# Optimization experiments

Hardware: AMD Instinct MI355X
Metric: run time of the kernel (lower is better)

The kernel has to match this reference:

```python
import jax, jax.numpy as jnp
import numpy as np

N_DIM = 256
NHIDDEN = 256
NLAYERS = 4
LAMDA = 0.5
ALPHA = 0.1
MODAL_WEIGHT = 1.0
N_SPEAKERS = 2
B_DIA = 100   # number of dialogues
L_DIA = 40    # utterances per dialogue
N_UTT = B_DIA * L_DIA


def _cos_sim_blocks(x, B, L):
    # per-dialogue cosine-similarity blocks: x [N, d] -> [B, L, L]
    xb = x.reshape(B, L, -1)
    xn = xb / jnp.linalg.norm(xb, axis=-1, keepdims=True)
    cos = jnp.einsum('bid,bjd->bij', xn, xn) * 0.99999
    return 1.0 - jnp.arccos(cos) / jnp.pi


def setup_inputs() -> dict:
    key = jax.random.key(0)
    ks = jax.random.split(key, 8)
    return {
        'a': jax.random.normal(ks[0], (N_UTT, N_DIM), jnp.float32),
        'v': jax.random.normal(ks[1], (N_UTT, N_DIM), jnp.float32),
        'l': jax.random.normal(ks[2], (N_UTT, N_DIM), jnp.float32),
        'qmask': jax.random.uniform(ks[3], (L_DIA, B_DIA, N_SPEAKERS), jnp.float32),
        'spk_emb': jax.random.normal(ks[4], (N_SPEAKERS, N_DIM), jnp.float32) * 0.02,
        'W0': jax.random.normal(ks[5], (N_DIM, NHIDDEN), jnp.float32) / np.sqrt(N_DIM).astype(np.float32),
        'b0': jnp.zeros((NHIDDEN,), jnp.float32),
        'Wconvs': jax.random.normal(ks[6], (NLAYERS, NHIDDEN, NHIDDEN), jnp.float32) / np.sqrt(NHIDDEN).astype(np.float32),
        'dia_len_each': L_DIA,
        'n_dialogues': B_DIA,
    }


def reference(a, v, l, qmask, spk_emb, W0, b0, Wconvs, dia_len_each, n_dialogues):
    B, L = n_dialogues, dia_len_each
    N = B * L
    M = 3  # modals 'avl'

    # --- speaker embedding added to text modality (use_speaker) ---
    # torch.cat([qmask[:x, i, :] for i, x in enumerate(dia_len)]) with equal lengths
    q = jnp.transpose(qmask, (1, 0, 2)).reshape(N, -1)   # [N, n_speakers]
    spk_idx = jnp.argmax(q, axis=-1)                      # [N]
    l = l + spk_emb[spk_idx]

    feats = [a, v, l]
    normed = [f / jnp.linalg.norm(f, axis=-1, keepdims=True) for f in feats]

    # --- create_big_adj: block-diag per-modal cosine-sim blocks + cross-modal diagonals ---
    adj = jnp.zeros((M * N, M * N), jnp.float32)
    idx = jnp.arange(N).reshape(B, L)
    rows = idx[:, :, None]   # [B, L, 1]
    cols = idx[:, None, :]   # [B, 1, L]
    ar = jnp.arange(N)
    for m in range(M):
        sim = _cos_sim_blocks(feats[m], B, L)            # [B, L, L]
        adj = adj.at[m * N + rows, m * N + cols].set(sim)
    for m in range(M):
        for n in range(M):
            if m == n:
                continue
            cs = jnp.sum(normed[m] * normed[n], axis=-1) * 0.99999
            dia_sim = 1.0 - jnp.arccos(cs) / jnp.pi
            adj = adj.at[m * N + ar, n * N + ar].set(dia_sim * MODAL_WEIGHT)
    d = jnp.sum(adj, axis=1)
    dinv = d ** -0.5
    adj = adj * dinv[:, None] * dinv[None, :]            # D^-1/2 A D^-1/2

    # --- GCNII_lyc propagation (eval mode, variant=False, no dropout) ---
    x = jnp.concatenate(feats, axis=0)                   # [3N, n_dim]
    h0 = jax.nn.relu(x @ W0 + b0)
    h = h0
    for i in range(NLAYERS):
        theta = float(np.log(LAMDA / (i + 1) + 1.0))
        hi = adj @ h
        support = (1.0 - ALPHA) * hi + ALPHA * h0
        h = jax.nn.relu(theta * (support @ Wconvs[i]) + (1.0 - theta) * support)
    feat = jnp.concatenate([x, h], axis=-1)              # use_residue

    # regroup modalities per utterance: [N, 3*(n_dim+nhidden)]
    out = jnp.concatenate([feat[:N], feat[N:2 * N], feat[2 * N:3 * N]], axis=-1)
    return out
```

## Files before the change

kernel.cpp:

```cpp
#include <hip/hip_runtime.h>
#include <hip/hip_bf16.h>

#define N_UTT 4000
#define NDIM 256
#define B_DIA 100
#define L_DIA 40
#define NLAYERS 4

typedef __attribute__((ext_vector_type(8))) short short8;
typedef __attribute__((ext_vector_type(4))) float f32x4;

union bfpk4 { __hip_bfloat16 h[4]; uint2 u; };

static __device__ __forceinline__ float bf2f(__hip_bfloat16 h) {
  union { float f; unsigned u; } x;
  x.u = ((unsigned)*(unsigned short*)&h) << 16;
  return x.f;
}

__global__ void k_wt(const float* __restrict__ W0, const float* __restrict__ Wc,
                     __hip_bfloat16* __restrict__ Wt) {
  int k0 = blockIdx.x * 64, n0 = blockIdx.y * 64, g = blockIdx.z;
  int t = threadIdx.x;
  const float* src = (g == 0) ? W0 : (Wc + (g - 1) * NDIM * NDIM);
  __shared__ float tile[64][65];
  #pragma unroll
  for (int it = 0; it < 16; it++) {
    int e = t + 256 * it;
    int row = e >> 6, col = e & 63;
    tile[row][col] = src[(k0 + row) * NDIM + n0 + col];
  }
  __syncthreads();
  #pragma unroll
  for (int it = 0; it < 16; it++) {
    int e = t + 256 * it;
    int row = e >> 6, col = e & 63;
    Wt[(g * NDIM + n0 + row) * NDIM + k0 + col] = __float2bfloat16(tile[col][row]);
  }
}

__global__ __launch_bounds__(512, 1) void k_main(
    const float* __restrict__ a, const float* __restrict__ v,
    const float* __restrict__ lf, const float* __restrict__ qmask,
    const float* __restrict__ spk, const float* __restrict__ b0,
    const __hip_bfloat16* __restrict__ Wt, float* __restrict__ out) {
  __shared__ __hip_bfloat16 xls[3][L_DIA][264];
  __shared__ __hip_bfloat16 hls[3][NDIM][L_DIA];
  __shared__ __hip_bfloat16 sext[3][L_DIA][136];
  __shared__ float invn[120];
  __shared__ float dinv[120];
  __shared__ float psum[120][4];

  int b = blockIdx.x;
  int t = threadIdx.x;
  int w = t >> 6, ln = t & 63;
  int l15 = ln & 15, lk = (ln >> 4) * 8;
  const float inv_pi = 0.31830988618379067f;

  int arows[3], cols[2];
  #pragma unroll
  for (int rt = 0; rt < 3; rt++) {
    int rr_ = rt * 16 + l15;
    arows[rt] = (rr_ < L_DIA) ? rr_ : (L_DIA - 1);
  }
  #pragma unroll
  for (int c = 0; c < 2; c++) cols[c] = w * 32 + c * 16 + l15;

  {
    unsigned int* sz = (unsigned int*)&sext[0][0][0];
    #pragma unroll
    for (int e = t; e < 3 * L_DIA * 136 / 2; e += 512) sz[e] = 0u;
  }
  for (int e = t; e < 120 * 64; e += 512) {
    int r = e >> 6, c4 = e & 63;
    int m = r / L_DIA, p = r - m * L_DIA;
    int i = b * L_DIA + p;
    float4 val;
    if (m == 0)      val = ((const float4*)a)[i * 64 + c4];
    else if (m == 1) val = ((const float4*)v)[i * 64 + c4];
    else {
      val = ((const float4*)lf)[i * 64 + c4];
      float q0 = qmask[(p * B_DIA + b) * 2 + 0];
      float q1 = qmask[(p * B_DIA + b) * 2 + 1];
      int s = (q1 > q0) ? 1 : 0;
      float4 sv = ((const float4*)spk)[s * 64 + c4];
      val.x += sv.x; val.y += sv.y; val.z += sv.z; val.w += sv.w;
    }
    ((float4*)out)[i * 384 + m * 128 + c4] = val;
    bfpk4 pk;
    pk.h[0] = __float2bfloat16(val.x); pk.h[1] = __float2bfloat16(val.y);
    pk.h[2] = __float2bfloat16(val.z); pk.h[3] = __float2bfloat16(val.w);
    *(uint2*)&xls[m][p][c4 * 4] = pk.u;
  }
  __syncthreads();

  if (t < 480) {
    int r = t >> 2, q4 = t & 3;
    int m = r / L_DIA, p = r - m * L_DIA;
    float s = 0.f;
    #pragma unroll
    for (int jj = 0; jj < 8; jj++) {
      short8 vv = *(const short8*)&xls[m][p][q4 * 64 + jj * 8];
      #pragma unroll
      for (int e = 0; e < 8; e++) {
        union { float f; unsigned u; } x;
        x.u = ((unsigned)(unsigned short)vv[e]) << 16;
        s += x.f * x.f;
      }
    }
    psum[r][q4] = s;
  }
  __syncthreads();
  if (t < 120) invn[t] = rsqrtf(psum[t][0] + psum[t][1] + psum[t][2] + psum[t][3]);
  __syncthreads();

  if (w < 3) {
    int mA = w;
    f32x4 sacc[3][3];
    #pragma unroll
    for (int rt = 0; rt < 3; rt++)
      #pragma unroll
      for (int ct = 0; ct < 3; ct++) sacc[rt][ct] = (f32x4){0.f,0.f,0.f,0.f};
    #pragma unroll
    for (int k0 = 0; k0 < NDIM; k0 += 32) {
      short8 fr[3];
      #pragma unroll
      for (int rt = 0; rt < 3; rt++)
        fr[rt] = *(const short8*)&xls[mA][arows[rt]][k0 + lk];
      #pragma unroll
      for (int rt = 0; rt < 3; rt++)
        #pragma unroll
        for (int ct = 0; ct < 3; ct++)
          sacc[rt][ct] = __builtin_amdgcn_mfma_f32_16x16x32_bf16(fr[rt], fr[ct], sacc[rt][ct], 0, 0, 0);
    }
    #pragma unroll
    for (int rt = 0; rt < 3; rt++)
      #pragma unroll
      for (int ct = 0; ct < 3; ct++)
        #pragma unroll
        for (int rr = 0; rr < 4; rr++) {
          int row = rt * 16 + (ln >> 4) * 4 + rr;
          int col = ct * 16 + l15;
          if (row < L_DIA && col < L_DIA) {
            float cs = sacc[rt][ct][rr] * invn[mA * 40 + row] * invn[mA * 40 + col] * 0.99999f;
            cs = fminf(fmaxf(cs, -1.f), 1.f);
            sext[mA][row][col] = __float2bfloat16(1.f - acosf(cs) * inv_pi);
          }
        }
  } else if (w < 6) {
    int pi = w - 3;
    int mA = (pi == 2) ? 1 : 0, mB = (pi == 0) ? 1 : 2;
    int slotA = (pi == 0) ? 40 : 80, slotB = (pi == 2) ? 80 : 40;
    f32x4 dacc[3];
    #pragma unroll
    for (int rt = 0; rt < 3; rt++) dacc[rt] = (f32x4){0.f,0.f,0.f,0.f};
    #pragma unroll
    for (int k0 = 0; k0 < NDIM; k0 += 32) {
      short8 frA[3], frB[3];
      #pragma unroll
      for (int rt = 0; rt < 3; rt++) {
        frA[rt] = *(const short8*)&xls[mA][arows[rt]][k0 + lk];
        frB[rt] = *(const short8*)&xls[mB][arows[rt]][k0 + lk];
      }
      #pragma unroll
      for (int rt = 0; rt < 3; rt++)
        dacc[rt] = __builtin_amdgcn_mfma_f32_16x16x32_bf16(frA[rt], frB[rt], dacc[rt], 0, 0, 0);
    }
    #pragma unroll
    for (int rt = 0; rt < 3; rt++)
      #pragma unroll
      for (int rr = 0; rr < 4; rr++) {
        int row = rt * 16 + (ln >> 4) * 4 + rr;
        if (l15 == ((ln >> 4) * 4 + rr) && row < L_DIA) {
          float cs = dacc[rt][rr] * invn[mA * 40 + row] * invn[mB * 40 + row] * 0.99999f;
          cs = fminf(fmaxf(cs, -1.f), 1.f);
          __hip_bfloat16 vv = __float2bfloat16(1.f - acosf(cs) * inv_pi);
          sext[mA][row][slotA + row] = vv;
          sext[mB][row][slotB + row] = vv;
        }
      }
  }
  __syncthreads();

  if (t < 120) {
    int m = t / 40, p = t - m * 40;
    float d = 0.f;
    #pragma unroll 10
    for (int q = 0; q < 40; q++) d += bf2f(sext[m][p][q]);
    d += bf2f(sext[m][p][40 + p]) + bf2f(sext[m][p][80 + p]);
    dinv[t] = rsqrtf(d);
  }
  __syncthreads();
  for (int e = t; e < 5040; e += 512) {
    if (e < 4800) {
      int m = e / 1600, rem = e - m * 1600;
      int p = rem / 40, q = rem - p * 40;
      sext[m][p][q] = __float2bfloat16(
          bf2f(sext[m][p][q]) * 0.9f * dinv[m * 40 + p] * dinv[m * 40 + q]);
    } else {
      int idx = e - 4800;
      int m = idx / 80, j = idx - m * 80;
      int which = j / 40, p = j - which * 40;
      int pmx = which ? ((m == 2) ? 1 : 2) : ((m == 0) ? 1 : 0);
      int k = 40 * (1 + which) + p;
      sext[m][p][k] = __float2bfloat16(
          bf2f(sext[m][p][k]) * 0.9f * dinv[m * 40 + p] * dinv[pmx * 40 + p]);
    }
  }
  __syncthreads();

  uint2 h0r[9][2];
  {
    f32x4 acc[9][2];
    #pragma unroll
    for (int s = 0; s < 9; s++)
      #pragma unroll
      for (int c = 0; c < 2; c++) acc[s][c] = (f32x4){0.f,0.f,0.f,0.f};
    #pragma unroll
    for (int k0 = 0; k0 < NDIM; k0 += 32) {
      short8 bfw[2];
      #pragma unroll
      for (int c = 0; c < 2; c++)
        bfw[c] = *(const short8*)&Wt[cols[c] * NDIM + k0 + lk];
      short8 af[9];
      #pragma unroll
      for (int s = 0; s < 9; s++)
        af[s] = *(const short8*)&xls[s / 3][arows[s % 3]][k0 + lk];
      #pragma unroll
      for (int s = 0; s < 9; s++)
        #pragma unroll
        for (int c = 0; c < 2; c++)
          acc[s][c] = __builtin_amdgcn_mfma_f32_16x16x32_bf16(af[s], bfw[c], acc[s][c], 0, 0, 0);
    }
    #pragma unroll
    for (int s = 0; s < 9; s++) {
      int p0 = (s % 3) * 16 + (ln >> 4) * 4;
      #pragma unroll
      for (int c = 0; c < 2; c++) {
        float bias = b0[cols[c]];
        bfpk4 pk;
        #pragma unroll
        for (int rr = 0; rr < 4; rr++)
          pk.h[rr] = __float2bfloat16(fmaxf(acc[s][c][rr] + bias, 0.f));
        h0r[s][c] = pk.u;
        if (p0 < L_DIA) *(uint2*)&hls[s / 3][cols[c]][p0] = pk.u;
      }
    }
  }
  __syncthreads();

  const float thetas[NLAYERS] = {0.40546510810816438f, 0.22314355131420976f,
                                 0.15415067982725836f, 0.11778303565638346f};
  #pragma unroll
  for (int li = 0; li < NLAYERS; li++) {
    float th = thetas[li], onemt = 1.f - th;
    const __hip_bfloat16* Wl = Wt + (li + 1) * NDIM * NDIM;

    {
      f32x4 acc[9][2];
      #pragma unroll
      for (int s = 0; s < 9; s++)
        #pragma unroll
        for (int c = 0; c < 2; c++) acc[s][c] = (f32x4){0.f,0.f,0.f,0.f};
      #pragma unroll
      for (int j = 0; j < 4; j++) {
        short8 bfv[3][2];
        #pragma unroll
        for (int mm = 0; mm < 3; mm++) {
          int pm0 = (mm == 0) ? 1 : 0, pm1 = (mm == 2) ? 1 : 2;
          int kk = j * 32 + lk;
          int srcm, brow;
          if (kk < 40)       { srcm = mm;  brow = kk; }
          else if (kk < 80)  { srcm = pm0; brow = kk - 40; }
          else if (kk < 120) { srcm = pm1; brow = kk - 80; }
          else               { srcm = pm1; brow = 32; }
          #pragma unroll
          for (int c = 0; c < 2; c++)
            bfv[mm][c] = *(const short8*)&hls[srcm][cols[c]][brow];
        }
        short8 af[9];
        #pragma unroll
        for (int s = 0; s < 9; s++)
          af[s] = *(const short8*)&sext[s / 3][arows[s % 3]][j * 32 + lk];
        #pragma unroll
        for (int s = 0; s < 9; s++)
          #pragma unroll
          for (int c = 0; c < 2; c++)
            acc[s][c] = __builtin_amdgcn_mfma_f32_16x16x32_bf16(af[s], bfv[s / 3][c], acc[s][c], 0, 0, 0);
      }
      #pragma unroll
      for (int s = 0; s < 9; s++) {
        int p0 = (s % 3) * 16 + (ln >> 4) * 4;
        #pragma unroll
        for (int c = 0; c < 2; c++) {
          bfpk4 h0p; h0p.u = h0r[s][c];
          if (p0 < L_DIA) {
            #pragma unroll
            for (int rr = 0; rr < 4; rr++)
              xls[s / 3][p0 + rr][cols[c]] =
                  __float2bfloat16(acc[s][c][rr] + 0.1f * bf2f(h0p.h[rr]));
          }
        }
      }
    }
    __syncthreads();

    {
      f32x4 o[9][2];
      #pragma unroll
      for (int s = 0; s < 9; s++)
        #pragma unroll
        for (int c = 0; c < 2; c++) o[s][c] = (f32x4){0.f,0.f,0.f,0.f};
      #pragma unroll
      for (int k0 = 0; k0 < NDIM; k0 += 32) {
        short8 bfw[2];
        #pragma unroll
        for (int c = 0; c < 2; c++)
          bfw[c] = *(const short8*)&Wl[cols[c] * NDIM + k0 + lk];
        short8 af[9];
        #pragma unroll
        for (int s = 0; s < 9; s++)
          af[s] = *(const short8*)&xls[s / 3][arows[s % 3]][k0 + lk];
        #pragma unroll
        for (int s = 0; s < 9; s++)
          #pragma unroll
          for (int c = 0; c < 2; c++)
            o[s][c] = __builtin_amdgcn_mfma_f32_16x16x32_bf16(af[s], bfw[c], o[s][c], 0, 0, 0);
      }
      #pragma unroll
      for (int s = 0; s < 9; s++) {
        int m = s / 3;
        int p0 = (s % 3) * 16 + (ln >> 4) * 4;
        if (p0 >= L_DIA) continue;
        #pragma unroll
        for (int c = 0; c < 2; c++) {
          int col = cols[c];
          if (li < NLAYERS - 1) {
            bfpk4 pk;
            #pragma unroll
            for (int rr = 0; rr < 4; rr++) {
              float supv = bf2f(xls[m][p0 + rr][col]);
              pk.h[rr] = __float2bfloat16(fmaxf(th * o[s][c][rr] + onemt * supv, 0.f));
            }
            *(uint2*)&hls[m][col][p0] = pk.u;
          } else {
            #pragma unroll
            for (int rr = 0; rr < 4; rr++) {
              float supv = bf2f(xls[m][p0 + rr][col]);
              out[(b * L_DIA + p0 + rr) * 1536 + m * 512 + 256 + col] =
                  fmaxf(th * o[s][c][rr] + onemt * supv, 0.f);
            }
          }
        }
      }
    }
    __syncthreads();
  }
}

extern "C" void kernel_launch(void* const* d_in, const int* in_sizes, int n_in,
                              void* d_out, int out_size, void* d_ws, size_t ws_size,
                              hipStream_t stream) {
  const float* a     = (const float*)d_in[0];
  const float* v     = (const float*)d_in[1];
  const float* lf    = (const float*)d_in[2];
  const float* qmask = (const float*)d_in[3];
  const float* spk   = (const float*)d_in[4];
  const float* W0    = (const float*)d_in[5];
  const float* b0    = (const float*)d_in[6];
  const float* Wc    = (const float*)d_in[7];
  float* out = (float*)d_out;

  __hip_bfloat16* Wt = (__hip_bfloat16*)d_ws;

  k_wt<<<dim3(4, 4, 5), 256, 0, stream>>>(W0, Wc, Wt);
  k_main<<<B_DIA, 512, 0, stream>>>(a, v, lf, qmask, spk, b0, Wt, out);
}
```

Before: 63.63 us.

## Split row-tiles across two wave groups with 64-column tiles per wave

```diff
diff --git a/kernel.cpp b/kernel.cpp
--- a/kernel.cpp
+++ b/kernel.cpp
@@ -57,14 +57,20 @@
   int l15 = ln & 15, lk = (ln >> 4) * 8;
   const float inv_pi = 0.31830988618379067f;
 
-  int arows[3], cols[2];
+  int sgrp = w >> 2;
+  int cw = w & 3;
+  int sbase = sgrp ? 5 : 0;
+  int scnt  = sgrp ? 4 : 5;
+  int mlist0 = sgrp ? 1 : 0, mlist1 = sgrp ? 2 : 1;
+
+  int arows[3], cols[4];
   #pragma unroll
   for (int rt = 0; rt < 3; rt++) {
     int rr_ = rt * 16 + l15;
     arows[rt] = (rr_ < L_DIA) ? rr_ : (L_DIA - 1);
   }
   #pragma unroll
-  for (int c = 0; c < 2; c++) cols[c] = w * 32 + c * 16 + l15;
+  for (int c = 0; c < 4; c++) cols[c] = cw * 64 + c * 16 + l15;
 
   {
     unsigned int* sz = (unsigned int*)&sext[0][0][0];
@@ -209,40 +215,46 @@
   }
   __syncthreads();
 
-  uint2 h0r[9][2];
+  uint2 h0r[5][4];
   {
-    f32x4 acc[9][2];
-    #pragma unroll
-    for (int s = 0; s < 9; s++)
-      #pragma unroll
-      for (int c = 0; c < 2; c++) acc[s][c] = (f32x4){0.f,0.f,0.f,0.f};
+    f32x4 acc[5][4];
+    #pragma unroll
+    for (int si = 0; si < 5; si++)
+      #pragma unroll
+      for (int c = 0; c < 4; c++) acc[si][c] = (f32x4){0.f,0.f,0.f,0.f};
     #pragma unroll
     for (int k0 = 0; k0 < NDIM; k0 += 32) {
-      short8 bfw[2];
-      #pragma unroll
-      for (int c = 0; c < 2; c++)
+      short8 bfw[4];
+      #pragma unroll
+      for (int c = 0; c < 4; c++)
         bfw[c] = *(const short8*)&Wt[cols[c] * NDIM + k0 + lk];
-      short8 af[9];
-      #pragma unroll
-      for (int s = 0; s < 9; s++)
-        af[s] = *(const short8*)&xls[s / 3][arows[s % 3]][k0 + lk];
-      #pragma unroll
-      for (int s = 0; s < 9; s++)
-        #pragma unroll
-        for (int c = 0; c < 2; c++)
-          acc[s][c] = __builtin_amdgcn_mfma_f32_16x16x32_bf16(af[s], bfw[c], acc[s][c], 0, 0, 0);
-    }
-    #pragma unroll
-    for (int s = 0; s < 9; s++) {
+      short8 af[5];
+      #pragma unroll
+      for (int si = 0; si < 5; si++)
+        if (si < scnt) {
+          int s = sbase + si;
+          af[si] = *(const short8*)&xls[s / 3][arows[s % 3]][k0 + lk];
+        }
+      #pragma unroll
+      for (int si = 0; si < 5; si++)
+        if (si < scnt)
+          #pragma unroll
+          for (int c = 0; c < 4; c++)
+            acc[si][c] = __builtin_amdgcn_mfma_f32_16x16x32_bf16(af[si], bfw[c], acc[si][c], 0, 0, 0);
+    }
+    #pragma unroll
+    for (int si = 0; si < 5; si++) {
+      if (si >= scnt) continue;
+      int s = sbase + si;
       int p0 = (s % 3) * 16 + (ln >> 4) * 4;
       #pragma unroll
-      for (int c = 0; c < 2; c++) {
+      for (int c = 0; c < 4; c++) {
         float bias = b0[cols[c]];
         bfpk4 pk;
         #pragma unroll
         for (int rr = 0; rr < 4; rr++)
-          pk.h[rr] = __float2bfloat16(fmaxf(acc[s][c][rr] + bias, 0.f));
-        h0r[s][c] = pk.u;
+          pk.h[rr] = __float2bfloat16(fmaxf(acc[si][c][rr] + bias, 0.f));
+        h0r[si][c] = pk.u;
         if (p0 < L_DIA) *(uint2*)&hls[s / 3][cols[c]][p0] = pk.u;
       }
     }
@@ -255,50 +267,64 @@
   for (int li = 0; li < NLAYERS; li++) {
     float th = thetas[li], onemt = 1.f - th;
     const __hip_bfloat16* Wl = Wt + (li + 1) * NDIM * NDIM;
+    uint2 supb[5][4];
 
     {
-      f32x4 acc[9][2];
-      #pragma unroll
-      for (int s = 0; s < 9; s++)
-        #pragma unroll
-        for (int c = 0; c < 2; c++) acc[s][c] = (f32x4){0.f,0.f,0.f,0.f};
+      f32x4 acc[5][4];
+      #pragma unroll
+      for (int si = 0; si < 5; si++)
+        #pragma unroll
+        for (int c = 0; c < 4; c++) acc[si][c] = (f32x4){0.f,0.f,0.f,0.f};
       #pragma unroll
       for (int j = 0; j < 4; j++) {
-        short8 bfv[3][2];
-        #pragma unroll
-        for (int mm = 0; mm < 3; mm++) {
+        int kk = j * 32 + lk;
+        short8 bfv[2][4];
+        #pragma unroll
+        for (int mi = 0; mi < 2; mi++) {
+          int mm = mi ? mlist1 : mlist0;
           int pm0 = (mm == 0) ? 1 : 0, pm1 = (mm == 2) ? 1 : 2;
-          int kk = j * 32 + lk;
           int srcm, brow;
           if (kk < 40)       { srcm = mm;  brow = kk; }
           else if (kk < 80)  { srcm = pm0; brow = kk - 40; }
           else if (kk < 120) { srcm = pm1; brow = kk - 80; }
           else               { srcm = pm1; brow = 32; }
           #pragma unroll
-          for (int c = 0; c < 2; c++)
-            bfv[mm][c] = *(const short8*)&hls[srcm][cols[c]][brow];
-        }
-        short8 af[9];
-        #pragma unroll
-        for (int s = 0; s < 9; s++)
-          af[s] = *(const short8*)&sext[s / 3][arows[s % 3]][j * 32 + lk];
-        #pragma unroll
-        for (int s = 0; s < 9; s++)
+          for (int c = 0; c < 4; c++)
+            bfv[mi][c] = *(const short8*)&hls[srcm][cols[c]][brow];
+        }
+        short8 af[5];
+        #pragma unroll
+        for (int si = 0; si < 5; si++)
+          if (si < scnt) {
+            int s = sbase + si;
+            af[si] = *(const short8*)&sext[s / 3][arows[s % 3]][j * 32 + lk];
+          }
+        #pragma unroll
+        for (int si = 0; si < 5; si++)
+          if (si < scnt) {
+            int mi = (((sbase + si) / 3) == mlist0) ? 0 : 1;
+            #pragma unroll
+            for (int c = 0; c < 4; c++)
+              acc[si][c] = __builtin_amdgcn_mfma_f32_16x16x32_bf16(af[si], bfv[mi][c], acc[si][c], 0, 0, 0);
+          }
+      }
+      #pragma unroll
+      for (int si = 0; si < 5; si++) {
+        if (si >= scnt) continue;
+        int s = sbase + si, m = s / 3;
+        int p0 = (s % 3) * 16 + (ln >> 4) * 4;
+        #pragma unroll
+        for (int c = 0; c < 4; c++) {
+          bfpk4 h0p; h0p.u = h0r[si][c];
+          bfpk4 pk;
           #pragma unroll
-          for (int c = 0; c < 2; c++)
-            acc[s][c] = __builtin_amdgcn_mfma_f32_16x16x32_bf16(af[s], bfv[s / 3][c], acc[s][c], 0, 0, 0);
-      }
-      #pragma unroll
-      for (int s = 0; s < 9; s++) {
-        int p0 = (s % 3) * 16 + (ln >> 4) * 4;
-        #pragma unroll
-        for (int c = 0; c < 2; c++) {
-          bfpk4 h0p; h0p.u = h0r[s][c];
+          for (int rr = 0; rr < 4; rr++)
+            pk.h[rr] = __float2bfloat16(acc[si][c][rr] + 0.1f * bf2f(h0p.h[rr]));
+          supb[si][c] = pk.u;
           if (p0 < L_DIA) {
             #pragma unroll
             for (int rr = 0; rr < 4; rr++)
-              xls[s / 3][p0 + rr][cols[c]] =
-                  __float2bfloat16(acc[s][c][rr] + 0.1f * bf2f(h0p.h[rr]));
+              xls[m][p0 + rr][cols[c]] = pk.h[rr];
           }
         }
       }
@@ -306,50 +332,52 @@
     __syncthreads();
 
     {
-      f32x4 o[9][2];
-      #pragma unroll
-      for (int s = 0; s < 9; s++)
-        #pragma unroll
-        for (int c = 0; c < 2; c++) o[s][c] = (f32x4){0.f,0.f,0.f,0.f};
+      f32x4 o[5][4];
+      #pragma unroll
+      for (int si = 0; si < 5; si++)
+        #pragma unroll
+        for (int c = 0; c < 4; c++) o[si][c] = (f32x4){0.f,0.f,0.f,0.f};
       #pragma unroll
       for (int k0 = 0; k0 < NDIM; k0 += 32) {
-        short8 bfw[2];
-        #pragma unroll
-        for (int c = 0; c < 2; c++)
+        short8 bfw[4];
+        #pragma unroll
+        for (int c = 0; c < 4; c++)
           bfw[c] = *(const short8*)&Wl[cols[c] * NDIM + k0 + lk];
-        short8 af[9];
-        #pragma unroll
-        for (int s = 0; s < 9; s++)
-          af[s] = *(const short8*)&xls[s / 3][arows[s % 3]][k0 + lk];
-        #pragma unroll
-        for (int s = 0; s < 9; s++)
-          #pragma unroll
-          for (int c = 0; c < 2; c++)
-            o[s][c] = __builtin_amdgcn_mfma_f32_16x16x32_bf16(af[s], bfw[c], o[s][c], 0, 0, 0);
-      }
-      #pragma unroll
-      for (int s = 0; s < 9; s++) {
-        int m = s / 3;
+        short8 af[5];
+        #pragma unroll
+        for (int si = 0; si < 5; si++)
+          if (si < scnt) {
+            int s = sbase + si;
+            af[si] = *(const short8*)&xls[s / 3][arows[s % 3]][k0 + lk];
+          }
+        #pragma unroll
+        for (int si = 0; si < 5; si++)
+          if (si < scnt)
+            #pragma unroll
+            for (int c = 0; c < 4; c++)
+              o[si][c] = __builtin_amdgcn_mfma_f32_16x16x32_bf16(af[si], bfw[c], o[si][c], 0, 0, 0);
+      }
+      #pragma unroll
+      for (int si = 0; si < 5; si++) {
+        if (si >= scnt) continue;
+        int s = sbase + si, m = s / 3;
         int p0 = (s % 3) * 16 + (ln >> 4) * 4;
         if (p0 >= L_DIA) continue;
         #pragma unroll
-        for (int c = 0; c < 2; c++) {
-          int col = cols[c];
+        for (int c = 0; c < 4; c++) {
+          bfpk4 sp; sp.u = supb[si][c];
           if (li < NLAYERS - 1) {
             bfpk4 pk;
             #pragma unroll
-            for (int rr = 0; rr < 4; rr++) {
-              float supv = bf2f(xls[m][p0 + rr][col]);
-              pk.h[rr] = __float2bfloat16(fmaxf(th * o[s][c][rr] + onemt * supv, 0.f));
-            }
-            *(uint2*)&hls[m][col][p0] = pk.u;
+            for (int rr = 0; rr < 4; rr++)
+              pk.h[rr] = __float2bfloat16(
+                  fmaxf(th * o[si][c][rr] + onemt * bf2f(sp.h[rr]), 0.f));
+            *(uint2*)&hls[m][cols[c]][p0] = pk.u;
           } else {
             #pragma unroll
-            for (int rr = 0; rr < 4; rr++) {
-              float supv = bf2f(xls[m][p0 + rr][col]);
-              out[(b * L_DIA + p0 + rr) * 1536 + m * 512 + 256 + col] =
-                  fmaxf(th * o[s][c][rr] + onemt * supv, 0.f);
-            }
+            for (int rr = 0; rr < 4; rr++)
+              out[(b * L_DIA + p0 + rr) * 1536 + m * 512 + 256 + cols[c]] =
+                  fmaxf(th * o[si][c][rr] + onemt * bf2f(sp.h[rr]), 0.f);
           }
         }
       }
```

After: 138.5 us. 2.18x slower.

## Use 12 waves per block, splitting work by modality and column group

Applied to the files above, without the earlier changes.

```diff
diff --git a/kernel.cpp b/kernel.cpp
--- a/kernel.cpp
+++ b/kernel.cpp
@@ -6,6 +6,7 @@
 #define B_DIA 100
 #define L_DIA 40
 #define NLAYERS 4
+#define NT 768
 
 typedef __attribute__((ext_vector_type(8))) short short8;
 typedef __attribute__((ext_vector_type(4))) float f32x4;
@@ -39,7 +40,7 @@
   }
 }
 
-__global__ __launch_bounds__(512, 1) void k_main(
+__global__ __launch_bounds__(NT, 3) void k_main(
     const float* __restrict__ a, const float* __restrict__ v,
     const float* __restrict__ lf, const float* __restrict__ qmask,
     const float* __restrict__ spk, const float* __restrict__ b0,
@@ -55,23 +56,28 @@
   int t = threadIdx.x;
   int w = t >> 6, ln = t & 63;
   int l15 = ln & 15, lk = (ln >> 4) * 8;
+  int hi4 = (ln >> 4) * 4;
   const float inv_pi = 0.31830988618379067f;
 
-  int arows[3], cols[2];
+  int mg = w >> 2;
+  int cg = w & 3;
+  int pm0 = (mg == 0) ? 1 : 0;
+  int pm1 = (mg == 2) ? 1 : 2;
+
+  int arows[3], cols[4];
   #pragma unroll
   for (int rt = 0; rt < 3; rt++) {
     int rr_ = rt * 16 + l15;
     arows[rt] = (rr_ < L_DIA) ? rr_ : (L_DIA - 1);
   }
   #pragma unroll
-  for (int c = 0; c < 2; c++) cols[c] = w * 32 + c * 16 + l15;
+  for (int c = 0; c < 4; c++) cols[c] = cg * 64 + c * 16 + l15;
 
   {
     unsigned int* sz = (unsigned int*)&sext[0][0][0];
-    #pragma unroll
-    for (int e = t; e < 3 * L_DIA * 136 / 2; e += 512) sz[e] = 0u;
-  }
-  for (int e = t; e < 120 * 64; e += 512) {
+    for (int e = t; e < 3 * L_DIA * 136 / 2; e += NT) sz[e] = 0u;
+  }
+  for (int e = t; e < 120 * 64; e += NT) {
     int r = e >> 6, c4 = e & 63;
     int m = r / L_DIA, p = r - m * L_DIA;
     int i = b * L_DIA + p;
@@ -139,7 +145,7 @@
       for (int ct = 0; ct < 3; ct++)
         #pragma unroll
         for (int rr = 0; rr < 4; rr++) {
-          int row = rt * 16 + (ln >> 4) * 4 + rr;
+          int row = rt * 16 + hi4 + rr;
           int col = ct * 16 + l15;
           if (row < L_DIA && col < L_DIA) {
             float cs = sacc[rt][ct][rr] * invn[mA * 40 + row] * invn[mA * 40 + col] * 0.99999f;
@@ -170,8 +176,8 @@
     for (int rt = 0; rt < 3; rt++)
       #pragma unroll
       for (int rr = 0; rr < 4; rr++) {
-        int row = rt * 16 + (ln >> 4) * 4 + rr;
-        if (l15 == ((ln >> 4) * 4 + rr) && row < L_DIA) {
+        int row = rt * 16 + hi4 + rr;
+        if (l15 == (hi4 + rr) && row < L_DIA) {
           float cs = dacc[rt][rr] * invn[mA * 40 + row] * invn[mB * 40 + row] * 0.99999f;
           cs = fminf(fmaxf(cs, -1.f), 1.f);
           __hip_bfloat16 vv = __float2bfloat16(1.f - acosf(cs) * inv_pi);
@@ -191,7 +197,7 @@
     dinv[t] = rsqrtf(d);
   }
   __syncthreads();
-  for (int e = t; e < 5040; e += 512) {
+  for (int e = t; e < 5040; e += NT) {
     if (e < 4800) {
       int m = e / 1600, rem = e - m * 1600;
       int p = rem / 40, q = rem - p * 40;
@@ -209,41 +215,41 @@
   }
   __syncthreads();
 
-  uint2 h0r[9][2];
+  uint2 h0r[3][4];
   {
-    f32x4 acc[9][2];
-    #pragma unroll
-    for (int s = 0; s < 9; s++)
-      #pragma unroll
-      for (int c = 0; c < 2; c++) acc[s][c] = (f32x4){0.f,0.f,0.f,0.f};
+    f32x4 acc[3][4];
+    #pragma unroll
+    for (int rt = 0; rt < 3; rt++)
+      #pragma unroll
+      for (int c = 0; c < 4; c++) acc[rt][c] = (f32x4){0.f,0.f,0.f,0.f};
     #pragma unroll
     for (int k0 = 0; k0 < NDIM; k0 += 32) {
-      short8 bfw[2];
-      #pragma unroll
-      for (int c = 0; c < 2; c++)
+      short8 bfw[4];
+      #pragma unroll
+      for (int c = 0; c < 4; c++)
         bfw[c] = *(const short8*)&Wt[cols[c] * NDIM + k0 + lk];
-      short8 af[9];
-      #pragma unroll
-      for (int s = 0; s < 9; s++)
-        af[s] = *(const short8*)&xls[s / 3][arows[s % 3]][k0 + lk];
-      #pragma unroll
-      for (int s = 0; s < 9; s++)
-        #pragma unroll
-        for (int c = 0; c < 2; c++)
-          acc[s][c] = __builtin_amdgcn_mfma_f32_16x16x32_bf16(af[s], bfw[c], acc[s][c], 0, 0, 0);
-    }
-    #pragma unroll
-    for (int s = 0; s < 9; s++) {
-      int p0 = (s % 3) * 16 + (ln >> 4) * 4;
-      #pragma unroll
-      for (int c = 0; c < 2; c++) {
+      short8 af[3];
+      #pragma unroll
+      for (int rt = 0; rt < 3; rt++)
+        af[rt] = *(const short8*)&xls[mg][arows[rt]][k0 + lk];
+      #pragma unroll
+      for (int rt = 0; rt < 3; rt++)
+        #pragma unroll
+        for (int c = 0; c < 4; c++)
+          acc[rt][c] = __builtin_amdgcn_mfma_f32_16x16x32_bf16(af[rt], bfw[c], acc[rt][c], 0, 0, 0);
+    }
+    #pragma unroll
+    for (int rt = 0; rt < 3; rt++) {
+      int p0 = rt * 16 + hi4;
+      #pragma unroll
+      for (int c = 0; c < 4; c++) {
         float bias = b0[cols[c]];
         bfpk4 pk;
         #pragma unroll
         for (int rr = 0; rr < 4; rr++)
-          pk.h[rr] = __float2bfloat16(fmaxf(acc[s][c][rr] + bias, 0.f));
-        h0r[s][c] = pk.u;
-        if (p0 < L_DIA) *(uint2*)&hls[s / 3][cols[c]][p0] = pk.u;
+          pk.h[rr] = __float2bfloat16(fmaxf(acc[rt][c][rr] + bias, 0.f));
+        h0r[rt][c] = pk.u;
+        if (p0 < L_DIA) *(uint2*)&hls[mg][cols[c]][p0] = pk.u;
       }
     }
   }
@@ -257,48 +263,44 @@
     const __hip_bfloat16* Wl = Wt + (li + 1) * NDIM * NDIM;
 
     {
-      f32x4 acc[9][2];
-      #pragma unroll
-      for (int s = 0; s < 9; s++)
-        #pragma unroll
-        for (int c = 0; c < 2; c++) acc[s][c] = (f32x4){0.f,0.f,0.f,0.f};
+      f32x4 acc[3][4];
+      #pragma unroll
+      for (int rt = 0; rt < 3; rt++)
+        #pragma unroll
+        for (int c = 0; c < 4; c++) acc[rt][c] = (f32x4){0.f,0.f,0.f,0.f};
       #pragma unroll
       for (int j = 0; j < 4; j++) {
-        short8 bfv[3][2];
-        #pragma unroll
-        for (int mm = 0; mm < 3; mm++) {
-          int pm0 = (mm == 0) ? 1 : 0, pm1 = (mm == 2) ? 1 : 2;
-          int kk = j * 32 + lk;
-          int srcm, brow;
-          if (kk < 40)       { srcm = mm;  brow = kk; }
-          else if (kk < 80)  { srcm = pm0; brow = kk - 40; }
-          else if (kk < 120) { srcm = pm1; brow = kk - 80; }
-          else               { srcm = pm1; brow = 32; }
+        int kk = j * 32 + lk;
+        int srcm, brow;
+        if (kk < 40)       { srcm = mg;  brow = kk; }
+        else if (kk < 80)  { srcm = pm0; brow = kk - 40; }
+        else if (kk < 120) { srcm = pm1; brow = kk - 80; }
+        else               { srcm = pm1; brow = 32; }
+        short8 bfv[4];
+        #pragma unroll
+        for (int c = 0; c < 4; c++)
+          bfv[c] = *(const short8*)&hls[srcm][cols[c]][brow];
+        short8 af[3];
+        #pragma unroll
+        for (int rt = 0; rt < 3; rt++)
+          af[rt] = *(const short8*)&sext[mg][arows[rt]][j * 32 + lk];
+        #pragma unroll
+        for (int rt = 0; rt < 3; rt++)
           #pragma unroll
-          for (int c = 0; c < 2; c++)
-            bfv[mm][c] = *(const short8*)&hls[srcm][cols[c]][brow];
-        }
-        short8 af[9];
-        #pragma unroll
-        for (int s = 0; s < 9; s++)
-          af[s] = *(const short8*)&sext[s / 3][arows[s % 3]][j * 32 + lk];
-        #pragma unroll
-        for (int s = 0; s < 9; s++)
+          for (int c = 0; c < 4; c++)
+            acc[rt][c] = __builtin_amdgcn_mfma_f32_16x16x32_bf16(af[rt], bfv[c], acc[rt][c], 0, 0, 0);
+      }
+      #pragma unroll
+      for (int rt = 0; rt < 3; rt++) {
+        int p0 = rt * 16 + hi4;
+        if (p0 < L_DIA) {
           #pragma unroll
-          for (int c = 0; c < 2; c++)
-            acc[s][c] = __builtin_amdgcn_mfma_f32_16x16x32_bf16(af[s], bfv[s / 3][c], acc[s][c], 0, 0, 0);
-      }
-      #pragma unroll
-      for (int s = 0; s < 9; s++) {
-        int p0 = (s % 3) * 16 + (ln >> 4) * 4;
-        #pragma unroll
-        for (int c = 0; c < 2; c++) {
-          bfpk4 h0p; h0p.u = h0r[s][c];
-          if (p0 < L_DIA) {
+          for (int c = 0; c < 4; c++) {
+            bfpk4 h0p; h0p.u = h0r[rt][c];
             #pragma unroll
             for (int rr = 0; rr < 4; rr++)
-              xls[s / 3][p0 + rr][cols[c]] =
-                  __float2bfloat16(acc[s][c][rr] + 0.1f * bf2f(h0p.h[rr]));
+              xls[mg][p0 + rr][cols[c]] =
+                  __float2bfloat16(acc[rt][c][rr] + 0.1f * bf2f(h0p.h[rr]));
           }
         }
       }
@@ -306,49 +308,48 @@
     __syncthreads();
 
     {
-      f32x4 o[9][2];
-      #pragma unroll
-      for (int s = 0; s < 9; s++)
-        #pragma unroll
-        for (int c = 0; c < 2; c++) o[s][c] = (f32x4){0.f,0.f,0.f,0.f};
+      f32x4 o[3][4];
+      #pragma unroll
+      for (int rt = 0; rt < 3; rt++)
+        #pragma unroll
+        for (int c = 0; c < 4; c++) o[rt][c] = (f32x4){0.f,0.f,0.f,0.f};
       #pragma unroll
       for (int k0 = 0; k0 < NDIM; k0 += 32) {
-        short8 bfw[2];
-        #pragma unroll
-        for (int c = 0; c < 2; c++)
+        short8 bfw[4];
+        #pragma unroll
+        for (int c = 0; c < 4; c++)
           bfw[c] = *(const short8*)&Wl[cols[c] * NDIM + k0 + lk];
-        short8 af[9];
-        #pragma unroll
-        for (int s = 0; s < 9; s++)
-          af[s] = *(const short8*)&xls[s / 3][arows[s % 3]][k0 + lk];
-        #pragma unroll
-        for (int s = 0; s < 9; s++)
+        short8 af[3];
+        #pragma unroll
+        for (int rt = 0; rt < 3; rt++)
+          af[rt] = *(const short8*)&xls[mg][arows[rt]][k0 + lk];
+        #pragma unroll
+        for (int rt = 0; rt < 3; rt++)
           #pragma unroll
-          for (int c = 0; c < 2; c++)
-            o[s][c] = __builtin_amdgcn_mfma_f32_16x16x32_bf16(af[s], bfw[c], o[s][c], 0, 0, 0);
-      }
-      #pragma unroll
-      for (int s = 0; s < 9; s++) {
-        int m = s / 3;
-        int p0 = (s % 3) * 16 + (ln >> 4) * 4;
+          for (int c = 0; c < 4; c++)
+            o[rt][c] = __builtin_amdgcn_mfma_f32_16x16x32_bf16(af[rt], bfw[c], o[rt][c], 0, 0, 0);
+      }
+      #pragma unroll
+      for (int rt = 0; rt < 3; rt++) {
+        int p0 = rt * 16 + hi4;
         if (p0 >= L_DIA) continue;
         #pragma unroll
-        for (int c = 0; c < 2; c++) {
+        for (int c = 0; c < 4; c++) {
           int col = cols[c];
           if (li < NLAYERS - 1) {
             bfpk4 pk;
             #pragma unroll
             for (int rr = 0; rr < 4; rr++) {
-              float supv = bf2f(xls[m][p0 + rr][col]);
-              pk.h[rr] = __float2bfloat16(fmaxf(th * o[s][c][rr] + onemt * supv, 0.f));
+              float supv = bf2f(xls[mg][p0 + rr][col]);
+              pk.h[rr] = __float2bfloat16(fmaxf(th * o[rt][c][rr] + onemt * supv, 0.f));
             }
-            *(uint2*)&hls[m][col][p0] = pk.u;
+            *(uint2*)&hls[mg][col][p0] = pk.u;
           } else {
             #pragma unroll
             for (int rr = 0; rr < 4; rr++) {
-              float supv = bf2f(xls[m][p0 + rr][col]);
-              out[(b * L_DIA + p0 + rr) * 1536 + m * 512 + 256 + col] =
-                  fmaxf(th * o[s][c][rr] + onemt * supv, 0.f);
+              float supv = bf2f(xls[mg][p0 + rr][col]);
+              out[(b * L_DIA + p0 + rr) * 1536 + mg * 512 + 256 + col] =
+                  fmaxf(th * o[rt][c][rr] + onemt * supv, 0.f);
             }
           }
         }
@@ -374,5 +375,5 @@
   __hip_bfloat16* Wt = (__hip_bfloat16*)d_ws;
 
   k_wt<<<dim3(4, 4, 5), 256, 0, stream>>>(W0, Wc, Wt);
-  k_main<<<B_DIA, 512, 0, stream>>>(a, v, lf, qmask, spk, b0, Wt, out);
+  k_main<<<B_DIA, NT, 0, stream>>>(a, v, lf, qmask, spk, b0, Wt, out);
 }
```

New measurement: 109.9 us. 72.8% more time.

## Retile dense GEMMs as 2x4 wave grid over 120 rows and spill h0 to global

Applied to the files above, without the earlier changes.

```diff
diff --git a/kernel.cpp b/kernel.cpp
--- a/kernel.cpp
+++ b/kernel.cpp
@@ -6,6 +6,7 @@
 #define B_DIA 100
 #define L_DIA 40
 #define NLAYERS 4
+#define XSTR 264
 
 typedef __attribute__((ext_vector_type(8))) short short8;
 typedef __attribute__((ext_vector_type(4))) float f32x4;
@@ -43,8 +44,9 @@
     const float* __restrict__ a, const float* __restrict__ v,
     const float* __restrict__ lf, const float* __restrict__ qmask,
     const float* __restrict__ spk, const float* __restrict__ b0,
-    const __hip_bfloat16* __restrict__ Wt, float* __restrict__ out) {
-  __shared__ __hip_bfloat16 xls[3][L_DIA][264];
+    const __hip_bfloat16* __restrict__ Wt, __hip_bfloat16* __restrict__ gh0,
+    float* __restrict__ out) {
+  __shared__ __hip_bfloat16 xls[120 * XSTR];
   __shared__ __hip_bfloat16 hls[3][NDIM][L_DIA];
   __shared__ __hip_bfloat16 sext[3][L_DIA][136];
   __shared__ float invn[120];
@@ -55,7 +57,9 @@
   int t = threadIdx.x;
   int w = t >> 6, ln = t & 63;
   int l15 = ln & 15, lk = (ln >> 4) * 8;
+  int hi4 = (ln >> 4) * 4;
   const float inv_pi = 0.31830988618379067f;
+  __hip_bfloat16* gh0d = gh0 + b * (3 * NDIM * 48);
 
   int arows[3], cols[2];
   #pragma unroll
@@ -65,6 +69,16 @@
   }
   #pragma unroll
   for (int c = 0; c < 2; c++) cols[c] = w * 32 + c * 16 + l15;
+
+  int rg = w >> 2, cg = w & 3;
+  int srows[4], cols4[4];
+  #pragma unroll
+  for (int i = 0; i < 4; i++) {
+    int rr_ = rg * 64 + i * 16 + l15;
+    srows[i] = (rr_ < 120) ? rr_ : 119;
+  }
+  #pragma unroll
+  for (int cc = 0; cc < 4; cc++) cols4[cc] = cg * 64 + cc * 16 + l15;
 
   {
     unsigned int* sz = (unsigned int*)&sext[0][0][0];
@@ -90,17 +104,16 @@
     bfpk4 pk;
     pk.h[0] = __float2bfloat16(val.x); pk.h[1] = __float2bfloat16(val.y);
     pk.h[2] = __float2bfloat16(val.z); pk.h[3] = __float2bfloat16(val.w);
-    *(uint2*)&xls[m][p][c4 * 4] = pk.u;
+    *(uint2*)&xls[r * XSTR + c4 * 4] = pk.u;
   }
   __syncthreads();
 
   if (t < 480) {
     int r = t >> 2, q4 = t & 3;
-    int m = r / L_DIA, p = r - m * L_DIA;
     float s = 0.f;
     #pragma unroll
     for (int jj = 0; jj < 8; jj++) {
-      short8 vv = *(const short8*)&xls[m][p][q4 * 64 + jj * 8];
+      short8 vv = *(const short8*)&xls[r * XSTR + q4 * 64 + jj * 8];
       #pragma unroll
       for (int e = 0; e < 8; e++) {
         union { float f; unsigned u; } x;
@@ -126,7 +139,7 @@
       short8 fr[3];
       #pragma unroll
       for (int rt = 0; rt < 3; rt++)
-        fr[rt] = *(const short8*)&xls[mA][arows[rt]][k0 + lk];
+        fr[rt] = *(const short8*)&xls[(mA * 40 + arows[rt]) * XSTR + k0 + lk];
       #pragma unroll
       for (int rt = 0; rt < 3; rt++)
         #pragma unroll
@@ -139,7 +152,7 @@
       for (int ct = 0; ct < 3; ct++)
         #pragma unroll
         for (int rr = 0; rr < 4; rr++) {
-          int row = rt * 16 + (ln >> 4) * 4 + rr;
+          int row = rt * 16 + hi4 + rr;
           int col = ct * 16 + l15;
           if (row < L_DIA && col < L_DIA) {
             float cs = sacc[rt][ct][rr] * invn[mA * 40 + row] * invn[mA * 40 + col] * 0.99999f;
@@ -159,8 +172,8 @@
       short8 frA[3], frB[3];
       #pragma unroll
       for (int rt = 0; rt < 3; rt++) {
-        frA[rt] = *(const short8*)&xls[mA][arows[rt]][k0 + lk];
-        frB[rt] = *(const short8*)&xls[mB][arows[rt]][k0 + lk];
+        frA[rt] = *(const short8*)&xls[(mA * 40 + arows[rt]) * XSTR + k0 + lk];
+        frB[rt] = *(const short8*)&xls[(mB * 40 + arows[rt]) * XSTR + k0 + lk];
       }
       #pragma unroll
       for (int rt = 0; rt < 3; rt++)
@@ -170,8 +183,8 @@
     for (int rt = 0; rt < 3; rt++)
       #pragma unroll
       for (int rr = 0; rr < 4; rr++) {
-        int row = rt * 16 + (ln >> 4) * 4 + rr;
-        if (l15 == ((ln >> 4) * 4 + rr) && row < L_DIA) {
+        int row = rt * 16 + hi4 + rr;
+        if (l15 == (hi4 + rr) && row < L_DIA) {
           float cs = dacc[rt][rr] * invn[mA * 40 + row] * invn[mB * 40 + row] * 0.99999f;
           cs = fminf(fmaxf(cs, -1.f), 1.f);
           __hip_bfloat16 vv = __float2bfloat16(1.f - acosf(cs) * inv_pi);
@@ -209,41 +222,43 @@
   }
   __syncthreads();
 
-  uint2 h0r[9][2];
   {
-    f32x4 acc[9][2];
-    #pragma unroll
-    for (int s = 0; s < 9; s++)
-      #pragma unroll
-      for (int c = 0; c < 2; c++) acc[s][c] = (f32x4){0.f,0.f,0.f,0.f};
+    f32x4 acc[4][4];
+    #pragma unroll
+    for (int i = 0; i < 4; i++)
+      #pragma unroll
+      for (int cc = 0; cc < 4; cc++) acc[i][cc] = (f32x4){0.f,0.f,0.f,0.f};
     #pragma unroll
     for (int k0 = 0; k0 < NDIM; k0 += 32) {
-      short8 bfw[2];
-      #pragma unroll
-      for (int c = 0; c < 2; c++)
-        bfw[c] = *(const short8*)&Wt[cols[c] * NDIM + k0 + lk];
-      short8 af[9];
-      #pragma unroll
-      for (int s = 0; s < 9; s++)
-        af[s] = *(const short8*)&xls[s / 3][arows[s % 3]][k0 + lk];
-      #pragma unroll
-      for (int s = 0; s < 9; s++)
-        #pragma unroll
-        for (int c = 0; c < 2; c++)
-          acc[s][c] = __builtin_amdgcn_mfma_f32_16x16x32_bf16(af[s], bfw[c], acc[s][c], 0, 0, 0);
-    }
-    #pragma unroll
-    for (int s = 0; s < 9; s++) {
-      int p0 = (s % 3) * 16 + (ln >> 4) * 4;
-      #pragma unroll
-      for (int c = 0; c < 2; c++) {
-        float bias = b0[cols[c]];
+      short8 bfw[4];
+      #pragma unroll
+      for (int cc = 0; cc < 4; cc++)
+        bfw[cc] = *(const short8*)&Wt[cols4[cc] * NDIM + k0 + lk];
+      short8 af[4];
+      #pragma unroll
+      for (int i = 0; i < 4; i++)
+        af[i] = *(const short8*)&xls[srows[i] * XSTR + k0 + lk];
+      #pragma unroll
+      for (int i = 0; i < 4; i++)
+        #pragma unroll
+        for (int cc = 0; cc < 4; cc++)
+          acc[i][cc] = __builtin_amdgcn_mfma_f32_16x16x32_bf16(af[i], bfw[cc], acc[i][cc], 0, 0, 0);
+    }
+    #pragma unroll
+    for (int i = 0; i < 4; i++) {
+      int row0 = rg * 64 + i * 16 + hi4;
+      if (row0 >= 120) continue;
+      int m = row0 / 40, p0 = row0 - m * 40;
+      #pragma unroll
+      for (int cc = 0; cc < 4; cc++) {
+        int col = cols4[cc];
+        float bias = b0[col];
         bfpk4 pk;
         #pragma unroll
         for (int rr = 0; rr < 4; rr++)
-          pk.h[rr] = __float2bfloat16(fmaxf(acc[s][c][rr] + bias, 0.f));
-        h0r[s][c] = pk.u;
-        if (p0 < L_DIA) *(uint2*)&hls[s / 3][cols[c]][p0] = pk.u;
+          pk.h[rr] = __float2bfloat16(fmaxf(acc[i][cc][rr] + bias, 0.f));
+        *(uint2*)&hls[m][col][p0] = pk.u;
+        *(uint2*)&gh0d[(m * NDIM + col) * 48 + p0] = pk.u;
       }
     }
   }
@@ -264,11 +279,11 @@
         for (int c = 0; c < 2; c++) acc[s][c] = (f32x4){0.f,0.f,0.f,0.f};
       #pragma unroll
       for (int j = 0; j < 4; j++) {
+        int kk = j * 32 + lk;
         short8 bfv[3][2];
         #pragma unroll
         for (int mm = 0; mm < 3; mm++) {
           int pm0 = (mm == 0) ? 1 : 0, pm1 = (mm == 2) ? 1 : 2;
-          int kk = j * 32 + lk;
           int srcm, brow;
           if (kk < 40)       { srcm = mm;  brow = kk; }
           else if (kk < 80)  { srcm = pm0; brow = kk - 40; }
@@ -290,14 +305,16 @@
       }
       #pragma unroll
       for (int s = 0; s < 9; s++) {
-        int p0 = (s % 3) * 16 + (ln >> 4) * 4;
-        #pragma unroll
-        for (int c = 0; c < 2; c++) {
-          bfpk4 h0p; h0p.u = h0r[s][c];
-          if (p0 < L_DIA) {
+        int m = s / 3;
+        int p0 = (s % 3) * 16 + hi4;
+        if (p0 < L_DIA) {
+          #pragma unroll
+          for (int c = 0; c < 2; c++) {
+            bfpk4 h0p;
+            h0p.u = *(const uint2*)&gh0d[(m * NDIM + cols[c]) * 48 + p0];
             #pragma unroll
             for (int rr = 0; rr < 4; rr++)
-              xls[s / 3][p0 + rr][cols[c]] =
+              xls[(m * 40 + p0 + rr) * XSTR + cols[c]] =
                   __float2bfloat16(acc[s][c][rr] + 0.1f * bf2f(h0p.h[rr]));
           }
         }
@@ -306,49 +323,49 @@
     __syncthreads();
 
     {
-      f32x4 o[9][2];
-      #pragma unroll
-      for (int s = 0; s < 9; s++)
-        #pragma unroll
-        for (int c = 0; c < 2; c++) o[s][c] = (f32x4){0.f,0.f,0.f,0.f};
+      f32x4 o[4][4];
+      #pragma unroll
+      for (int i = 0; i < 4; i++)
+        #pragma unroll
+        for (int cc = 0; cc < 4; cc++) o[i][cc] = (f32x4){0.f,0.f,0.f,0.f};
       #pragma unroll
       for (int k0 = 0; k0 < NDIM; k0 += 32) {
-        short8 bfw[2];
-        #pragma unroll
-        for (int c = 0; c < 2; c++)
-          bfw[c] = *(const short8*)&Wl[cols[c] * NDIM + k0 + lk];
-        short8 af[9];
-        #pragma unroll
-        for (int s = 0; s < 9; s++)
-          af[s] = *(const short8*)&xls[s / 3][arows[s % 3]][k0 + lk];
-        #pragma unroll
-        for (int s = 0; s < 9; s++)
+        short8 bfw[4];
+        #pragma unroll
+        for (int cc = 0; cc < 4; cc++)
+          bfw[cc] = *(const short8*)&Wl[cols4[cc] * NDIM + k0 + lk];
+        short8 af[4];
+        #pragma unroll
+        for (int i = 0; i < 4; i++)
+          af[i] = *(const short8*)&xls[srows[i] * XSTR + k0 + lk];
+        #pragma unroll
+        for (int i = 0; i < 4; i++)
           #pragma unroll
-          for (int c = 0; c < 2; c++)
-            o[s][c] = __builtin_amdgcn_mfma_f32_16x16x32_bf16(af[s], bfw[c], o[s][c], 0, 0, 0);
-      }
-      #pragma unroll
-      for (int s = 0; s < 9; s++) {
-        int m = s / 3;
-        int p0 = (s % 3) * 16 + (ln >> 4) * 4;
-        if (p0 >= L_DIA) continue;
-        #pragma unroll
-        for (int c = 0; c < 2; c++) {
-          int col = cols[c];
+          for (int cc = 0; cc < 4; cc++)
+            o[i][cc] = __builtin_amdgcn_mfma_f32_16x16x32_bf16(af[i], bfw[cc], o[i][cc], 0, 0, 0);
+      }
+      #pragma unroll
+      for (int i = 0; i < 4; i++) {
+        int row0 = rg * 64 + i * 16 + hi4;
+        if (row0 >= 120) continue;
+        int m = row0 / 40, p0 = row0 - m * 40;
+        #pragma unroll
+        for (int cc = 0; cc < 4; cc++) {
+          int col = cols4[cc];
           if (li < NLAYERS - 1) {
             bfpk4 pk;
             #pragma unroll
             for (int rr = 0; rr < 4; rr++) {
-              float supv = bf2f(xls[m][p0 + rr][col]);
-              pk.h[rr] = __float2bfloat16(fmaxf(th * o[s][c][rr] + onemt * supv, 0.f));
+              float supv = bf2f(xls[(row0 + rr) * XSTR + col]);
+              pk.h[rr] = __float2bfloat16(fmaxf(th * o[i][cc][rr] + onemt * supv, 0.f));
             }
             *(uint2*)&hls[m][col][p0] = pk.u;
           } else {
             #pragma unroll
             for (int rr = 0; rr < 4; rr++) {
-              float supv = bf2f(xls[m][p0 + rr][col]);
+              float supv = bf2f(xls[(row0 + rr) * XSTR + col]);
               out[(b * L_DIA + p0 + rr) * 1536 + m * 512 + 256 + col] =
-                  fmaxf(th * o[s][c][rr] + onemt * supv, 0.f);
+                  fmaxf(th * o[i][cc][rr] + onemt * supv, 0.f);
             }
           }
         }
@@ -371,8 +388,9 @@
   const float* Wc    = (const float*)d_in[7];
   float* out = (float*)d_out;
 
-  __hip_bfloat16* Wt = (__hip_bfloat16*)d_ws;
+  __hip_bfloat16* Wt  = (__hip_bfloat16*)d_ws;
+  __hip_bfloat16* gh0 = Wt + 5 * NDIM * NDIM;
 
   k_wt<<<dim3(4, 4, 5), 256, 0, stream>>>(W0, Wc, Wt);
-  k_main<<<B_DIA, 512, 0, stream>>>(a, v, lf, qmask, spk, b0, Wt, out);
+  k_main<<<B_DIA, 512, 0, stream>>>(a, v, lf, qmask, spk, b0, Wt, gh0, out);
 }
```

Measured after the change: 84.12 us. 1.32x slower.
